# Kernel optimization log

Measured on AMD Instinct MI355X. Metric: run time of the kernel, lower is better.

Reference implementation:

```python
import jax, jax.numpy as jnp
import numpy as np

D = 128      # d_model
H = 8        # n_heads
HD = D // H  # head_dim = 16
E = 256      # n_experts
R = 32       # kv_lora_rank
B, T = 4, 512
EPS = 1e-6


def _dense_init(k, fi, fo):
    s = float(1.0 / np.sqrt(fi))
    return jax.random.uniform(k, (fi, fo), minval=-s, maxval=s, dtype=jnp.float32)


def setup_inputs() -> dict:
    key = jax.random.key(0)
    ks = jax.random.split(key, 16)
    rng = np.random.RandomState(42)
    Q, _ = np.linalg.qr(rng.randn(D, D))
    glim = float(np.sqrt(6.0 / (D + D)))
    return {
        'x': jax.random.normal(ks[0], (B, T, D), dtype=jnp.float32),
        'g1': jnp.ones((D,), jnp.float32),
        'qW': _dense_init(ks[1], D, D), 'qb': jnp.zeros((D,), jnp.float32),
        'kdW': _dense_init(ks[2], D, R), 'kdb': jnp.zeros((R,), jnp.float32),
        'kuW': _dense_init(ks[3], R, 2 * D), 'kub': jnp.zeros((2 * D,), jnp.float32),
        'oW': _dense_init(ks[4], D, D), 'ob': jnp.zeros((D,), jnp.float32),
        'rot': jnp.asarray(Q, jnp.float32),
        'tq_scale': jnp.ones((D,), jnp.float32),
        's1W': _dense_init(ks[5], D, D), 's1b': jnp.zeros((D,), jnp.float32),
        's2W': _dense_init(ks[6], D, D), 's2b': jnp.zeros((D,), jnp.float32),
        'g2': jnp.ones((D,), jnp.float32),
        'gateW': _dense_init(ks[7], D, E), 'gateb': jnp.zeros((E,), jnp.float32),
        'expW': jax.random.uniform(ks[8], (E, D, D), minval=-glim, maxval=glim, dtype=jnp.float32),
        'm1W': _dense_init(ks[9], D, D), 'm1b': jnp.zeros((D,), jnp.float32),
        'm2W': _dense_init(ks[10], D, D), 'm2b': jnp.zeros((D,), jnp.float32),
    }


def _rmsnorm(x, g):
    return g * (x / jnp.sqrt(jnp.mean(x * x, axis=-1, keepdims=True) + EPS))


def _swiglu(x, w1, b1, w2, b2):
    gate = x @ w1 + b1
    return gate * jax.nn.sigmoid(gate) * (x @ w2 + b2)


def _mla(x, qW, qb, kdW, kdb, kuW, kub, oW, ob):
    b, t = x.shape[0], x.shape[1]
    q = (x @ qW + qb).reshape(b, t, H, HD)
    kv = ((x @ kdW + kdb) @ kuW + kub).reshape(b, t, H, 2 * HD)
    k, v = jnp.split(kv, 2, axis=-1)
    q = jax.nn.elu(q) + 1.0
    k = jax.nn.elu(k) + 1.0
    # linear attention: context[b,h,d,e] = sum_t k[b,t,h,d] v[b,t,h,e]
    context = jnp.einsum('bthd,bthe->bhde', k, v)
    out = jnp.einsum('bthd,bhde->bthe', q, context)
    k_sum = jnp.sum(k, axis=1)  # [b,h,d]
    z = 1.0 / (jnp.einsum('bthd,bhd->bth', q, k_sum) + EPS)
    out = out * z[..., None]
    return out.reshape(b, t, D) @ oW + ob


def _turbo_quant(x, rot, scale):
    x = x @ rot
    mag = jnp.sqrt(jnp.mean(x * x, axis=-1, keepdims=True) + EPS)
    phase = x / mag
    qp = jnp.clip(phase * 127.0, -127.0, 127.0) / 127.0
    phase = jax.lax.stop_gradient(qp - phase) + phase  # straight-through
    return phase * mag * scale


def _moe(h, gateW, gateb, expW, m1W, m1b, m2W, m2b):
    gate_scores = jax.nn.softmax(h @ gateW + gateb, axis=-1)  # [B,T,E]
    top_vals, top_idx = jax.lax.top_k(gate_scores, 2)
    top_w = top_vals / (jnp.sum(top_vals, axis=-1, keepdims=True) + EPS)
    # dense all-expert compute as in the original module
    eo = jnp.einsum('btd,edo->bteo', h, expW)  # [B,T,E,D]
    mask = jnp.sum(jax.nn.one_hot(top_idx, E, dtype=h.dtype) * top_w[..., None], axis=2)  # [B,T,E]
    wavg = jnp.einsum('bteo,bte->bto', eo, mask)
    wavg = _swiglu(wavg, m1W, m1b, m2W, m2b)
    diff_sq = jnp.square(eo - wavg[:, :, None, :])
    wvar = jnp.einsum('bteo,bte->bto', diff_sq, mask)
    consensus = jnp.exp(-jnp.mean(wvar, axis=-1))  # [B,T]
    return wavg, consensus


def reference(x, g1, qW, qb, kdW, kdb, kuW, kub, oW, ob, rot, tq_scale,
              s1W, s1b, s2W, s2b, g2, gateW, gateb, expW, m1W, m1b, m2W, m2b):
    attn_out = _turbo_quant(_mla(_rmsnorm(x, g1), qW, qb, kdW, kdb, kuW, kub, oW, ob), rot, tq_scale)
    x = x + _swiglu(attn_out, s1W, s1b, s2W, s2b)
    moe_out, consensus = _moe(_rmsnorm(x, g2), gateW, gateb, expW, m1W, m1b, m2W, m2b)
    return x + moe_out, consensus
```

## Files before the change

kernel.cpp:

```cpp
#include <hip/hip_runtime.h>
#include <hip/hip_bf16.h>
#include <math.h>

static constexpr int Dd   = 128;
static constexpr int NH   = 8;
static constexpr int NE   = 256;
static constexpr int RR   = 32;
static constexpr int TT   = 512;
static constexpr int NTOK = 2048;
static constexpr int TPB  = 4;
static constexpr int SLOTS = 256;
#define EPSF 1e-6f

__device__ __forceinline__ float elu1(float v) { return v > 0.f ? v + 1.f : expf(v); }
__device__ __forceinline__ float sigm(float v) { return 1.f / (1.f + expf(-v)); }

__global__ __launch_bounds__(512) void k_pre(
    const float* __restrict__ x, const float* __restrict__ g1,
    const float* __restrict__ qW, const float* __restrict__ qb,
    const float* __restrict__ kdW, const float* __restrict__ kdb,
    const float* __restrict__ kuW, const float* __restrict__ kub,
    float* __restrict__ qbuf, float* __restrict__ kvbuf,
    float* __restrict__ ctx, float* __restrict__ ksum, int* __restrict__ cnt) {
  const int tid = threadIdx.x;
  const int j = tid & 127, g = tid >> 7;
  const int lane = tid & 63;
  const int n0 = blockIdx.x * TPB;

  __shared__ float4 h1T[128];
  __shared__ float4 part[3][128];
  __shared__ float4 kpart[8][32];
  __shared__ float4 kdT[32];
  __shared__ float4 kupart[256];
  __shared__ float4 rtmp[2];

  if (blockIdx.x == 0) {
    for (int i = tid; i < 32 * 256; i += 512) ctx[i] = 0.f;
    ksum[tid] = 0.f;
    if (tid < 256) cnt[tid] = 0;
  }

  float xv[4];
  if (tid < 128) {
    float v[4];
#pragma unroll
    for (int t = 0; t < 4; t++) { xv[t] = x[(n0 + t) * Dd + j]; v[t] = xv[t] * xv[t]; }
#pragma unroll
    for (int o = 32; o > 0; o >>= 1) {
#pragma unroll
      for (int t = 0; t < 4; t++) v[t] += __shfl_xor(v[t], o, 64);
    }
    if (lane == 0) rtmp[tid >> 6] = make_float4(v[0], v[1], v[2], v[3]);
  }
  __syncthreads();
  if (tid < 128) {
    float g1j = g1[j];
#pragma unroll
    for (int t = 0; t < 4; t++) {
      float ss = ((const float*)&rtmp[0])[t] + ((const float*)&rtmp[1])[t];
      ((float*)&h1T[j])[t] = g1j * xv[t] * rsqrtf(ss * (1.f / 128.f) + EPSF);
    }
  }
  __syncthreads();

  {
    float a0 = 0, a1 = 0, a2 = 0, a3 = 0;
    const float* Wp = qW + (g * 32) * Dd + j;
#pragma unroll 16
    for (int i = 0; i < 32; i++) {
      float4 h4 = h1T[g * 32 + i];
      float w = Wp[i * Dd];
      a0 += h4.x * w; a1 += h4.y * w; a2 += h4.z * w; a3 += h4.w * w;
    }
    if (g) part[g - 1][j] = make_float4(a0, a1, a2, a3);
    __syncthreads();
    if (g == 0) {
      float4 p0 = part[0][j], p1 = part[1][j], p2 = part[2][j];
      float bb = qb[j];
      qbuf[(n0 + 0) * Dd + j] = elu1(a0 + p0.x + p1.x + p2.x + bb);
      qbuf[(n0 + 1) * Dd + j] = elu1(a1 + p0.y + p1.y + p2.y + bb);
      qbuf[(n0 + 2) * Dd + j] = elu1(a2 + p0.z + p1.z + p2.z + bb);
      qbuf[(n0 + 3) * Dd + j] = elu1(a3 + p0.w + p1.w + p2.w + bb);
    }
    __syncthreads();
  }

  if (tid < 256) {
    int col = tid & 31, ksp = tid >> 5;
    float a0 = 0, a1 = 0, a2 = 0, a3 = 0;
    const float* Wp = kdW + (ksp * 16) * RR + col;
#pragma unroll
    for (int i = 0; i < 16; i++) {
      float4 h4 = h1T[ksp * 16 + i];
      float w = Wp[i * RR];
      a0 += h4.x * w; a1 += h4.y * w; a2 += h4.z * w; a3 += h4.w * w;
    }
    kpart[ksp][col] = make_float4(a0, a1, a2, a3);
  }
  __syncthreads();
  if (tid < 32) {
    float bb = kdb[tid];
    float s0 = bb, s1 = bb, s2 = bb, s3 = bb;
#pragma unroll
    for (int k = 0; k < 8; k++) {
      float4 p = kpart[k][tid];
      s0 += p.x; s1 += p.y; s2 += p.z; s3 += p.w;
    }
    kdT[tid] = make_float4(s0, s1, s2, s3);
  }
  __syncthreads();

  {
    int col = tid & 255, kh = tid >> 8;
    float a0 = 0, a1 = 0, a2 = 0, a3 = 0;
    const float* Wp = kuW + (kh * 16) * 256 + col;
#pragma unroll
    for (int r = 0; r < 16; r++) {
      float4 k4 = kdT[kh * 16 + r];
      float w = Wp[r * 256];
      a0 += k4.x * w; a1 += k4.y * w; a2 += k4.z * w; a3 += k4.w * w;
    }
    if (kh) kupart[col] = make_float4(a0, a1, a2, a3);
    __syncthreads();
    if (!kh) {
      float4 p = kupart[col];
      float bb = kub[col];
      bool isk = (col & 31) < 16;
      float v0 = a0 + p.x + bb, v1 = a1 + p.y + bb, v2 = a2 + p.z + bb, v3 = a3 + p.w + bb;
      kvbuf[(n0 + 0) * 256 + col] = isk ? elu1(v0) : v0;
      kvbuf[(n0 + 1) * 256 + col] = isk ? elu1(v1) : v1;
      kvbuf[(n0 + 2) * 256 + col] = isk ? elu1(v2) : v2;
      kvbuf[(n0 + 3) * 256 + col] = isk ? elu1(v3) : v3;
    }
  }
}

__global__ __launch_bounds__(256) void k_ctx(const float* __restrict__ kv,
                                             float* __restrict__ ctx,
                                             float* __restrict__ ksum,
                                             const float* __restrict__ oW,
                                             const float* __restrict__ ob,
                                             const float* __restrict__ rot,
                                             float* __restrict__ oR,
                                             float* __restrict__ bR) {
  const int blk = blockIdx.x;
  const int tid = threadIdx.x;
  if (blk < 256) {
    const int bh = blk >> 3, c = blk & 7;
    const int b = bh >> 3, h = bh & 7;
    const int d = tid >> 4, e = tid & 15;
    __shared__ float sh[64 * 32];
#pragma unroll
    for (int r = 0; r < 8; r++) {
      int lin = r * 256 + tid;
      int tok = lin >> 5, off = lin & 31;
      sh[lin] = kv[((b * TT + c * 64 + tok) * 256) + h * 32 + off];
    }
    __syncthreads();
    float acc = 0.f, ks = 0.f;
#pragma unroll 4
    for (int t = 0; t < 64; t++) {
      float kk = sh[t * 32 + d];
      acc += kk * sh[t * 32 + 16 + e];
      ks += kk;
    }
    atomicAdd(&ctx[bh * 256 + d * 16 + e], acc);
    if (e == 0) atomicAdd(&ksum[bh * 16 + d], ks);
  } else if (blk < 320) {
    int idx = (blk - 256) * 256 + tid;
    int row = idx >> 7, col = idx & 127;
    const float* ow = oW + row * 128;
    float acc = 0.f;
#pragma unroll 8
    for (int k = 0; k < 128; k++) acc += ow[k] * rot[k * 128 + col];
    oR[row * 128 + col] = acc;
  } else {
    if (tid < 128) {
      float acc = 0.f;
#pragma unroll 8
      for (int k = 0; k < 128; k++) acc += ob[k] * rot[k * 128 + tid];
      bR[tid] = acc;
    }
  }
}

__global__ __launch_bounds__(512) void k_mid(
    const float* __restrict__ x, const float* __restrict__ qbuf,
    const float* __restrict__ ctx, const float* __restrict__ ksum,
    const float* __restrict__ oR, const float* __restrict__ bR,
    const float* __restrict__ tqs,
    const float* __restrict__ s1W, const float* __restrict__ s1b,
    const float* __restrict__ s2W, const float* __restrict__ s2b,
    const float* __restrict__ g2, const float* __restrict__ gateW,
    const float* __restrict__ gateb,
    float* __restrict__ xnbuf, float* __restrict__ h2buf,
    float* __restrict__ gw, int* __restrict__ tokslot,
    int* __restrict__ slottok, int* __restrict__ cnt) {
  const int tid = threadIdx.x;
  const int j = tid & 127, g = tid >> 7;
  const int lane = tid & 63;
  const int n0 = blockIdx.x * TPB;
  const int b = n0 >> 9;

  __shared__ float4 bufA[128], bufB[128];
  __shared__ float4 part[3][128];
  __shared__ float4 gpart[256];
  __shared__ float4 rtmp[2];
  __shared__ float wvS[4][4]; __shared__ int wiS[4][4];
  __shared__ float zS[4][4];

  float xres[4];
  if (tid < 128) {
#pragma unroll
    for (int t = 0; t < 4; t++) xres[t] = x[(n0 + t) * Dd + j];
  }

  ((float*)&bufA[j])[g] = qbuf[(n0 + g) * Dd + j];
  __syncthreads();

  if (tid < 128) {
    int h = j >> 4, e = j & 15;
    const float* cpt = ctx + (b * NH + h) * 256;
    const float* kpt = ksum + (b * NH + h) * 16;
    float num[4] = {0, 0, 0, 0}, den[4] = {0, 0, 0, 0};
#pragma unroll
    for (int d = 0; d < 16; d++) {
      float cx = cpt[d * 16 + e], ks = kpt[d];
      float4 q4 = bufA[h * 16 + d];
      num[0] += q4.x * cx; num[1] += q4.y * cx; num[2] += q4.z * cx; num[3] += q4.w * cx;
      den[0] += q4.x * ks; den[1] += q4.y * ks; den[2] += q4.z * ks; den[3] += q4.w * ks;
    }
#pragma unroll
    for (int t = 0; t < 4; t++) ((float*)&bufB[j])[t] = num[t] / (den[t] + EPSF);
  }
  __syncthreads();

  {
    float a0 = 0, a1 = 0, a2 = 0, a3 = 0;
    const float* Wp = oR + (g * 32) * Dd + j;
#pragma unroll 16
    for (int i = 0; i < 32; i++) {
      float4 h4 = bufB[g * 32 + i];
      float w = Wp[i * Dd];
      a0 += h4.x * w; a1 += h4.y * w; a2 += h4.z * w; a3 += h4.w * w;
    }
    if (g) part[g - 1][j] = make_float4(a0, a1, a2, a3);
    __syncthreads();
    float tot[4];
    if (g == 0) {
      float4 p0 = part[0][j], p1 = part[1][j], p2 = part[2][j];
      float bb = bR[j];
      tot[0] = a0 + p0.x + p1.x + p2.x + bb; tot[1] = a1 + p0.y + p1.y + p2.y + bb;
      tot[2] = a2 + p0.z + p1.z + p2.z + bb; tot[3] = a3 + p0.w + p1.w + p2.w + bb;
      float v[4];
#pragma unroll
      for (int t = 0; t < 4; t++) v[t] = tot[t] * tot[t];
#pragma unroll
      for (int o = 32; o > 0; o >>= 1) {
#pragma unroll
        for (int t = 0; t < 4; t++) v[t] += __shfl_xor(v[t], o, 64);
      }
      if (lane == 0) rtmp[tid >> 6] = make_float4(v[0], v[1], v[2], v[3]);
    }
    __syncthreads();
    if (g == 0) {
      float scj = tqs[j];
#pragma unroll
      for (int t = 0; t < 4; t++) {
        float ss = ((const float*)&rtmp[0])[t] + ((const float*)&rtmp[1])[t];
        float mag = sqrtf(ss * (1.f / 128.f) + EPSF);
        float zc = fminf(fmaxf(tot[t], -mag), mag);
        ((float*)&bufA[j])[t] = zc * scj;
      }
    }
    __syncthreads();
  }

  {
    float a0 = 0, a1 = 0, a2 = 0, a3 = 0;
    const float* Wp = (g < 2 ? s1W : s2W) + ((g & 1) * 64) * Dd + j;
#pragma unroll 16
    for (int i = 0; i < 64; i++) {
      float4 h4 = bufA[(g & 1) * 64 + i];
      float w = Wp[i * Dd];
      a0 += h4.x * w; a1 += h4.y * w; a2 += h4.z * w; a3 += h4.w * w;
    }
    if (g) part[g - 1][j] = make_float4(a0, a1, a2, a3);
    __syncthreads();
    if (g == 0) {
      float b1 = s1b[j], b2 = s2b[j];
      float4 p0 = part[0][j], p1 = part[1][j], p2 = part[2][j];
      float gv[4], uv[4], xn[4], v[4];
      gv[0] = a0 + p0.x + b1; gv[1] = a1 + p0.y + b1;
      gv[2] = a2 + p0.z + b1; gv[3] = a3 + p0.w + b1;
      uv[0] = p1.x + p2.x + b2; uv[1] = p1.y + p2.y + b2;
      uv[2] = p1.z + p2.z + b2; uv[3] = p1.w + p2.w + b2;
      float g2j = g2[j];
#pragma unroll
      for (int t = 0; t < 4; t++) {
        xn[t] = xres[t] + gv[t] * sigm(gv[t]) * uv[t];
        xnbuf[(n0 + t) * Dd + j] = xn[t];
        ((float*)&bufB[j])[t] = g2j * xn[t];
        v[t] = xn[t] * xn[t];
      }
#pragma unroll
      for (int o = 32; o > 0; o >>= 1) {
#pragma unroll
        for (int t = 0; t < 4; t++) v[t] += __shfl_xor(v[t], o, 64);
      }
      if (lane == 0) rtmp[tid >> 6] = make_float4(v[0], v[1], v[2], v[3]);
    }
    __syncthreads();
  }

  float val[4];
  float r2[4];
  {
    int col = tid & 255, kh = tid >> 8;
    float a0 = 0, a1 = 0, a2 = 0, a3 = 0;
    const float* Wp = gateW + (kh * 64) * NE + col;
#pragma unroll 16
    for (int i = 0; i < 64; i++) {
      float4 h4 = bufB[kh * 64 + i];
      float w = Wp[i * NE];
      a0 += h4.x * w; a1 += h4.y * w; a2 += h4.z * w; a3 += h4.w * w;
    }
    if (kh) gpart[col] = make_float4(a0, a1, a2, a3);
    __syncthreads();
#pragma unroll
    for (int t = 0; t < 4; t++) {
      float ss = ((const float*)&rtmp[0])[t] + ((const float*)&rtmp[1])[t];
      r2[t] = rsqrtf(ss * (1.f / 128.f) + EPSF);
    }
    if (!kh) {
      float4 p = gpart[col];
      float bb = gateb[col];
      val[0] = (a0 + p.x) * r2[0] + bb; val[1] = (a1 + p.y) * r2[1] + bb;
      val[2] = (a2 + p.z) * r2[2] + bb; val[3] = (a3 + p.w) * r2[3] + bb;
    }
    if (tid < 128) {
#pragma unroll
      for (int t = 0; t < 4; t++)
        h2buf[(n0 + t) * Dd + j] = ((const float*)&bufB[j])[t] * r2[t];
    }
  }
  __syncthreads();

  float m1[4]; int i1[4];
  {
    if (tid < 256) {
      float bv[4]; int bi[4];
#pragma unroll
      for (int t = 0; t < 4; t++) { bv[t] = val[t]; bi[t] = tid; }
#pragma unroll
      for (int o = 32; o > 0; o >>= 1) {
#pragma unroll
        for (int t = 0; t < 4; t++) {
          float wv = __shfl_xor(bv[t], o, 64);
          int wi = __shfl_xor(bi[t], o, 64);
          if (wv > bv[t] || (wv == bv[t] && wi < bi[t])) { bv[t] = wv; bi[t] = wi; }
        }
      }
      if (lane == 0) {
#pragma unroll
        for (int t = 0; t < 4; t++) { wvS[tid >> 6][t] = bv[t]; wiS[tid >> 6][t] = bi[t]; }
      }
    }
    __syncthreads();
    if (tid < 256) {
#pragma unroll
      for (int t = 0; t < 4; t++) {
        m1[t] = wvS[0][t]; i1[t] = wiS[0][t];
#pragma unroll
        for (int w = 1; w < 4; w++) {
          float cv = wvS[w][t]; int ci = wiS[w][t];
          if (cv > m1[t] || (cv == m1[t] && ci < i1[t])) { m1[t] = cv; i1[t] = ci; }
        }
      }
    }
    __syncthreads();
  }
  float m2[4]; int i2[4];
  {
    if (tid < 256) {
      float bv[4]; int bi[4];
#pragma unroll
      for (int t = 0; t < 4; t++) {
        bv[t] = (tid == i1[t]) ? -INFINITY : val[t];
        bi[t] = tid;
      }
#pragma unroll
      for (int o = 32; o > 0; o >>= 1) {
#pragma unroll
        for (int t = 0; t < 4; t++) {
          float wv = __shfl_xor(bv[t], o, 64);
          int wi = __shfl_xor(bi[t], o, 64);
          if (wv > bv[t] || (wv == bv[t] && wi < bi[t])) { bv[t] = wv; bi[t] = wi; }
        }
      }
      if (lane == 0) {
#pragma unroll
        for (int t = 0; t < 4; t++) { wvS[tid >> 6][t] = bv[t]; wiS[tid >> 6][t] = bi[t]; }
      }
    }
    __syncthreads();
    if (tid < 256) {
#pragma unroll
      for (int t = 0; t < 4; t++) {
        m2[t] = wvS[0][t]; i2[t] = wiS[0][t];
#pragma unroll
        for (int w = 1; w < 4; w++) {
          float cv = wvS[w][t]; int ci = wiS[w][t];
          if (cv > m2[t] || (cv == m2[t] && ci < i2[t])) { m2[t] = cv; i2[t] = ci; }
        }
      }
    }
    __syncthreads();
  }
  {
    if (tid < 256) {
      float v[4];
#pragma unroll
      for (int t = 0; t < 4; t++) v[t] = expf(val[t] - m1[t]);
#pragma unroll
      for (int o = 32; o > 0; o >>= 1) {
#pragma unroll
        for (int t = 0; t < 4; t++) v[t] += __shfl_xor(v[t], o, 64);
      }
      if (lane == 0) {
#pragma unroll
        for (int t = 0; t < 4; t++) zS[tid >> 6][t] = v[t];
      }
    }
    __syncthreads();
  }
  if (tid < 4) {
    int t = tid, tok = n0 + t;
    float Z = zS[0][t] + zS[1][t] + zS[2][t] + zS[3][t];
    float p1 = 1.f / Z;
    float p2 = expf(m2[t] - m1[t]) / Z;
    float s = p1 + p2 + EPSF;
    int e1 = i1[t], e2 = i2[t];
    int s1 = atomicAdd(&cnt[e1], 1); if (s1 > SLOTS - 1) s1 = SLOTS - 1;
    int s2 = atomicAdd(&cnt[e2], 1); if (s2 > SLOTS - 1) s2 = SLOTS - 1;
    int sl1 = e1 * SLOTS + s1, sl2 = e2 * SLOTS + s2;
    slottok[sl1] = tok; slottok[sl2] = tok;
    tokslot[tok * 2] = sl1; tokslot[tok * 2 + 1] = sl2;
    gw[tok * 2] = p1 / s; gw[tok * 2 + 1] = p2 / s;
  }
}

__global__ __launch_bounds__(512) void k_exp(const float* __restrict__ h2buf,
                                             const int* __restrict__ slottok,
                                             const int* __restrict__ cnt,
                                             const float* __restrict__ expW,
                                             float* __restrict__ ybuf) {
  const int e = blockIdx.x;
  int n = cnt[e]; if (n > SLOTS) n = SLOTS;
  if (n == 0) return;
  const int base = e * SLOTS;
  const int tid = threadIdx.x;
  const int j = tid & 127, g = tid >> 7;
  __shared__ __align__(16) float hT[128 * 20];
  const float* Wp = expW + (size_t)e * Dd * Dd + j;
  for (int t0 = 0; t0 < n; t0 += 16) {
    int m = n - t0; if (m > 16) m = 16;
    __syncthreads();
    for (int tt = g; tt < m; tt += 4) {
      int tok = slottok[base + t0 + tt];
      hT[j * 20 + tt] = h2buf[tok * Dd + j];
    }
    __syncthreads();
    float acc[4] = {0, 0, 0, 0};
#pragma unroll 8
    for (int i = 0; i < 128; i++) {
      float w = Wp[i * Dd];
      float4 h4 = *(const float4*)&hT[i * 20 + g * 4];
      acc[0] += h4.x * w; acc[1] += h4.y * w; acc[2] += h4.z * w; acc[3] += h4.w * w;
    }
#pragma unroll
    for (int k = 0; k < 4; k++) {
      int tt = g * 4 + k;
      if (tt < m) ybuf[(size_t)(base + t0 + tt) * Dd + j] = acc[k];
    }
  }
}

__global__ __launch_bounds__(512) void k_post(
    const float* __restrict__ xnbuf, const float* __restrict__ ybuf,
    const int* __restrict__ tokslot, const float* __restrict__ gw,
    const float* __restrict__ m1W, const float* __restrict__ m1b,
    const float* __restrict__ m2W, const float* __restrict__ m2b,
    float* __restrict__ out) {
  const int tid = threadIdx.x;
  const int j = tid & 127, g = tid >> 7;
  const int lane = tid & 63;
  const int n0 = blockIdx.x * TPB;

  __shared__ float4 y1T[128], y2T[128], inT[128], sT[128];
  __shared__ float4 part[3][128];
  __shared__ float4 rtmp[2];
  __shared__ int sSlot[4][2];
  __shared__ float sWt[4][2];

  if (tid < 4) {
    sSlot[tid][0] = tokslot[(n0 + tid) * 2];
    sSlot[tid][1] = tokslot[(n0 + tid) * 2 + 1];
    sWt[tid][0] = gw[(n0 + tid) * 2];
    sWt[tid][1] = gw[(n0 + tid) * 2 + 1];
  }
  __syncthreads();

  {
    float y1 = ybuf[(size_t)sSlot[g][0] * Dd + j];
    float y2 = ybuf[(size_t)sSlot[g][1] * Dd + j];
    ((float*)&y1T[j])[g] = y1;
    ((float*)&y2T[j])[g] = y2;
    ((float*)&inT[j])[g] = sWt[g][0] * y1 + sWt[g][1] * y2;
  }
  __syncthreads();

  {
    float a0 = 0, a1 = 0, a2 = 0, a3 = 0;
    const float* Wp = (g < 2 ? m1W : m2W) + ((g & 1) * 64) * Dd + j;
#pragma unroll 16
    for (int i = 0; i < 64; i++) {
      float4 h4 = inT[(g & 1) * 64 + i];
      float w = Wp[i * Dd];
      a0 += h4.x * w; a1 += h4.y * w; a2 += h4.z * w; a3 += h4.w * w;
    }
    if (g) part[g - 1][j] = make_float4(a0, a1, a2, a3);
    __syncthreads();
    if (g == 0) {
      float b1 = m1b[j], b2 = m2b[j];
      float4 p0 = part[0][j], p1 = part[1][j], p2 = part[2][j];
      float gv[4], uv[4];
      gv[0] = a0 + p0.x + b1; gv[1] = a1 + p0.y + b1;
      gv[2] = a2 + p0.z + b1; gv[3] = a3 + p0.w + b1;
      uv[0] = p1.x + p2.x + b2; uv[1] = p1.y + p2.y + b2;
      uv[2] = p1.z + p2.z + b2; uv[3] = p1.w + p2.w + b2;
#pragma unroll
      for (int t = 0; t < 4; t++) {
        float sv = gv[t] * sigm(gv[t]) * uv[t];
        ((float*)&sT[j])[t] = sv;
        out[(n0 + t) * Dd + j] = xnbuf[(n0 + t) * Dd + j] + sv;
      }
    }
    __syncthreads();
  }

  if (tid < 128) {
    float v[4];
#pragma unroll
    for (int t = 0; t < 4; t++) {
      float sv = ((const float*)&sT[j])[t];
      float d1 = ((const float*)&y1T[j])[t] - sv;
      float d2 = ((const float*)&y2T[j])[t] - sv;
      v[t] = sWt[t][0] * d1 * d1 + sWt[t][1] * d2 * d2;
    }
#pragma unroll
    for (int o = 32; o > 0; o >>= 1) {
#pragma unroll
      for (int t = 0; t < 4; t++) v[t] += __shfl_xor(v[t], o, 64);
    }
    if (lane == 0) rtmp[tid >> 6] = make_float4(v[0], v[1], v[2], v[3]);
  }
  __syncthreads();
  if (tid < 4) {
    float s = ((const float*)&rtmp[0])[tid] + ((const float*)&rtmp[1])[tid];
    out[NTOK * Dd + n0 + tid] = expf(-s * (1.f / 128.f));
  }
}

extern "C" void kernel_launch(void* const* d_in, const int* in_sizes, int n_in,
                              void* d_out, int out_size, void* d_ws, size_t ws_size,
                              hipStream_t stream) {
  const float* x   = (const float*)d_in[0];
  const float* g1  = (const float*)d_in[1];
  const float* qW  = (const float*)d_in[2];
  const float* qb  = (const float*)d_in[3];
  const float* kdW = (const float*)d_in[4];
  const float* kdb = (const float*)d_in[5];
  const float* kuW = (const float*)d_in[6];
  const float* kub = (const float*)d_in[7];
  const float* oW  = (const float*)d_in[8];
  const float* ob  = (const float*)d_in[9];
  const float* rot = (const float*)d_in[10];
  const float* tqs = (const float*)d_in[11];
  const float* s1W = (const float*)d_in[12];
  const float* s1b = (const float*)d_in[13];
  const float* s2W = (const float*)d_in[14];
  const float* s2b = (const float*)d_in[15];
  const float* g2  = (const float*)d_in[16];
  const float* gW  = (const float*)d_in[17];
  const float* gb  = (const float*)d_in[18];
  const float* eW  = (const float*)d_in[19];
  const float* m1W = (const float*)d_in[20];
  const float* m1b = (const float*)d_in[21];
  const float* m2W = (const float*)d_in[22];
  const float* m2b = (const float*)d_in[23];
  float* out = (float*)d_out;
  float* ws  = (float*)d_ws;

  float* qbuf   = ws;
  float* kvbuf  = ws + 262144;
  float* ctx    = ws + 786432;
  float* ksum   = ws + 794624;
  float* h2buf  = ws + 795136;
  float* xnbuf  = ws + 1057280;
  float* gw     = ws + 1319424;
  float* oRb    = ws + 1323520;
  float* bRb    = ws + 1339904;
  int*   cnt     = (int*)(ws + 1373056);
  int*   tokslot = (int*)(ws + 1373312);
  int*   slottok = (int*)(ws + 1377408);
  float* ybuf   = ws + 1442944;

  k_pre<<<NTOK / TPB, 512, 0, stream>>>(x, g1, qW, qb, kdW, kdb, kuW, kub,
                                        qbuf, kvbuf, ctx, ksum, cnt);
  k_ctx<<<321, 256, 0, stream>>>(kvbuf, ctx, ksum, oW, ob, rot, oRb, bRb);
  k_mid<<<NTOK / TPB, 512, 0, stream>>>(x, qbuf, ctx, ksum, oRb, bRb, tqs,
                                        s1W, s1b, s2W, s2b, g2, gW, gb,
                                        xnbuf, h2buf, gw, tokslot, slottok, cnt);
  k_exp<<<NE, 512, 0, stream>>>(h2buf, slottok, cnt, eW, ybuf);
  k_post<<<NTOK / TPB, 512, 0, stream>>>(xnbuf, ybuf, tokslot, gw,
                                         m1W, m1b, m2W, m2b, out);
}
```

Measured before the change: 165.4 us.

## Fuse pipeline into two stages with per-token expert compute and in-block context accumulation

Five kernels become a zero kernel plus two fused stages. The linear-attention context and key sums are now accumulated with atomics straight from each block's K/V in shared memory, so the kvbuf round trip and the separate ctx kernel go away. The oW·rot precompute also moves into stage1. The MoE top-2 expert matmuls now run inside stage2 per 4-token block, loading weights by token instead of grouping tokens by expert. This drops the slot-scatter bookkeeping, the expert and post kernels, and the h2/xn/y buffers, but each block rereads full expert weight matrices with less reuse and issues many more atomics.

```diff
diff --git a/kernel.cpp b/kernel.cpp
--- a/kernel.cpp
+++ b/kernel.cpp
@@ -1,31 +1,38 @@
 #include <hip/hip_runtime.h>
-#include <hip/hip_bf16.h>
 #include <math.h>
 
-static constexpr int Dd   = 128;
-static constexpr int NH   = 8;
-static constexpr int NE   = 256;
-static constexpr int RR   = 32;
-static constexpr int TT   = 512;
-static constexpr int NTOK = 2048;
-static constexpr int TPB  = 4;
-static constexpr int SLOTS = 256;
+static constexpr int Dd    = 128;
+static constexpr int NH    = 8;
+static constexpr int NE    = 256;
+static constexpr int RR    = 32;
+static constexpr int NTOK  = 2048;
 #define EPSF 1e-6f
 
 __device__ __forceinline__ float elu1(float v) { return v > 0.f ? v + 1.f : expf(v); }
 __device__ __forceinline__ float sigm(float v) { return 1.f / (1.f + expf(-v)); }
 
-__global__ __launch_bounds__(512) void k_pre(
+__global__ __launch_bounds__(512) void k_zero(float* __restrict__ ctx,
+                                              float* __restrict__ ksum) {
+  int idx = blockIdx.x * 512 + threadIdx.x;
+  if (idx < 8192) ctx[idx] = 0.f;
+  else if (idx < 8704) ksum[idx - 8192] = 0.f;
+}
+
+__global__ __launch_bounds__(512) void k_stage1(
     const float* __restrict__ x, const float* __restrict__ g1,
     const float* __restrict__ qW, const float* __restrict__ qb,
     const float* __restrict__ kdW, const float* __restrict__ kdb,
     const float* __restrict__ kuW, const float* __restrict__ kub,
-    float* __restrict__ qbuf, float* __restrict__ kvbuf,
-    float* __restrict__ ctx, float* __restrict__ ksum, int* __restrict__ cnt) {
+    const float* __restrict__ oW, const float* __restrict__ ob,
+    const float* __restrict__ rot,
+    float* __restrict__ qbuf, float* __restrict__ ctx, float* __restrict__ ksum,
+    float* __restrict__ oR, float* __restrict__ bR) {
   const int tid = threadIdx.x;
+  const int bid = blockIdx.x;
   const int j = tid & 127, g = tid >> 7;
   const int lane = tid & 63;
-  const int n0 = blockIdx.x * TPB;
+  const int n0 = bid * 4;
+  const int b = bid >> 7;
 
   __shared__ float4 h1T[128];
   __shared__ float4 part[3][128];
@@ -33,12 +40,8 @@
   __shared__ float4 kdT[32];
   __shared__ float4 kupart[256];
   __shared__ float4 rtmp[2];
-
-  if (blockIdx.x == 0) {
-    for (int i = tid; i < 32 * 256; i += 512) ctx[i] = 0.f;
-    ksum[tid] = 0.f;
-    if (tid < 256) cnt[tid] = 0;
-  }
+  __shared__ __align__(16) float kS[8][16][4];
+  __shared__ __align__(16) float vS[8][16][4];
 
   float xv[4];
   if (tid < 128) {
@@ -125,66 +128,52 @@
     if (!kh) {
       float4 p = kupart[col];
       float bb = kub[col];
-      bool isk = (col & 31) < 16;
       float v0 = a0 + p.x + bb, v1 = a1 + p.y + bb, v2 = a2 + p.z + bb, v3 = a3 + p.w + bb;
-      kvbuf[(n0 + 0) * 256 + col] = isk ? elu1(v0) : v0;
-      kvbuf[(n0 + 1) * 256 + col] = isk ? elu1(v1) : v1;
-      kvbuf[(n0 + 2) * 256 + col] = isk ? elu1(v2) : v2;
-      kvbuf[(n0 + 3) * 256 + col] = isk ? elu1(v3) : v3;
-    }
-  }
-}
-
-__global__ __launch_bounds__(256) void k_ctx(const float* __restrict__ kv,
-                                             float* __restrict__ ctx,
-                                             float* __restrict__ ksum,
-                                             const float* __restrict__ oW,
-                                             const float* __restrict__ ob,
-                                             const float* __restrict__ rot,
-                                             float* __restrict__ oR,
-                                             float* __restrict__ bR) {
-  const int blk = blockIdx.x;
-  const int tid = threadIdx.x;
-  if (blk < 256) {
-    const int bh = blk >> 3, c = blk & 7;
-    const int b = bh >> 3, h = bh & 7;
-    const int d = tid >> 4, e = tid & 15;
-    __shared__ float sh[64 * 32];
-#pragma unroll
-    for (int r = 0; r < 8; r++) {
-      int lin = r * 256 + tid;
-      int tok = lin >> 5, off = lin & 31;
-      sh[lin] = kv[((b * TT + c * 64 + tok) * 256) + h * 32 + off];
-    }
-    __syncthreads();
-    float acc = 0.f, ks = 0.f;
-#pragma unroll 4
-    for (int t = 0; t < 64; t++) {
-      float kk = sh[t * 32 + d];
-      acc += kk * sh[t * 32 + 16 + e];
-      ks += kk;
-    }
-    atomicAdd(&ctx[bh * 256 + d * 16 + e], acc);
-    if (e == 0) atomicAdd(&ksum[bh * 16 + d], ks);
-  } else if (blk < 320) {
-    int idx = (blk - 256) * 256 + tid;
+      int h = col >> 5, off = col & 31;
+      if (off < 16) {
+        kS[h][off][0] = elu1(v0); kS[h][off][1] = elu1(v1);
+        kS[h][off][2] = elu1(v2); kS[h][off][3] = elu1(v3);
+      } else {
+        vS[h][off - 16][0] = v0; vS[h][off - 16][1] = v1;
+        vS[h][off - 16][2] = v2; vS[h][off - 16][3] = v3;
+      }
+    }
+  }
+  __syncthreads();
+
+  {
+    const int h = tid >> 6;
+    const int d = (tid >> 2) & 15;
+    const int e0 = (tid & 3) * 4;
+    const int bh = b * NH + h;
+    float4 k4 = *(const float4*)&kS[h][d][0];
+    float* cp = ctx + bh * 256 + d * 16 + e0;
+#pragma unroll
+    for (int ee = 0; ee < 4; ee++) {
+      float4 v4 = *(const float4*)&vS[h][e0 + ee][0];
+      atomicAdd(cp + ee, k4.x * v4.x + k4.y * v4.y + k4.z * v4.z + k4.w * v4.w);
+    }
+    if ((tid & 3) == 0)
+      atomicAdd(&ksum[bh * 16 + d], k4.x + k4.y + k4.z + k4.w);
+  }
+
+  if (bid < 32) {
+    int idx = bid * 512 + tid;
     int row = idx >> 7, col = idx & 127;
     const float* ow = oW + row * 128;
     float acc = 0.f;
 #pragma unroll 8
     for (int k = 0; k < 128; k++) acc += ow[k] * rot[k * 128 + col];
-    oR[row * 128 + col] = acc;
-  } else {
-    if (tid < 128) {
-      float acc = 0.f;
+    oR[idx] = acc;
+  } else if (bid == 32 && tid < 128) {
+    float acc = 0.f;
 #pragma unroll 8
-      for (int k = 0; k < 128; k++) acc += ob[k] * rot[k * 128 + tid];
-      bR[tid] = acc;
-    }
+    for (int k = 0; k < 128; k++) acc += ob[k] * rot[k * 128 + tid];
+    bR[tid] = acc;
   }
 }
 
-__global__ __launch_bounds__(512) void k_mid(
+__global__ __launch_bounds__(512) void k_stage2(
     const float* __restrict__ x, const float* __restrict__ qbuf,
     const float* __restrict__ ctx, const float* __restrict__ ksum,
     const float* __restrict__ oR, const float* __restrict__ bR,
@@ -192,14 +181,14 @@
     const float* __restrict__ s1W, const float* __restrict__ s1b,
     const float* __restrict__ s2W, const float* __restrict__ s2b,
     const float* __restrict__ g2, const float* __restrict__ gateW,
-    const float* __restrict__ gateb,
-    float* __restrict__ xnbuf, float* __restrict__ h2buf,
-    float* __restrict__ gw, int* __restrict__ tokslot,
-    int* __restrict__ slottok, int* __restrict__ cnt) {
+    const float* __restrict__ gateb, const float* __restrict__ expW,
+    const float* __restrict__ m1W, const float* __restrict__ m1b,
+    const float* __restrict__ m2W, const float* __restrict__ m2b,
+    float* __restrict__ out) {
   const int tid = threadIdx.x;
   const int j = tid & 127, g = tid >> 7;
   const int lane = tid & 63;
-  const int n0 = blockIdx.x * TPB;
+  const int n0 = blockIdx.x * 4;
   const int b = n0 >> 9;
 
   __shared__ float4 bufA[128], bufB[128];
@@ -208,6 +197,11 @@
   __shared__ float4 rtmp[2];
   __shared__ float wvS[4][4]; __shared__ int wiS[4][4];
   __shared__ float zS[4][4];
+  __shared__ float sWt[4][2]; __shared__ int sE[4][2];
+  __shared__ float h2T[128][4];
+  __shared__ float epS[8][4][128];
+  __shared__ float yT[8][128];
+  __shared__ float4 inT[128], sT[128];
 
   float xres[4];
   if (tid < 128) {
@@ -276,6 +270,7 @@
     __syncthreads();
   }
 
+  float xn[4] = {0.f, 0.f, 0.f, 0.f};
   {
     float a0 = 0, a1 = 0, a2 = 0, a3 = 0;
     const float* Wp = (g < 2 ? s1W : s2W) + ((g & 1) * 64) * Dd + j;
@@ -290,7 +285,7 @@
     if (g == 0) {
       float b1 = s1b[j], b2 = s2b[j];
       float4 p0 = part[0][j], p1 = part[1][j], p2 = part[2][j];
-      float gv[4], uv[4], xn[4], v[4];
+      float gv[4], uv[4], v[4];
       gv[0] = a0 + p0.x + b1; gv[1] = a1 + p0.y + b1;
       gv[2] = a2 + p0.z + b1; gv[3] = a3 + p0.w + b1;
       uv[0] = p1.x + p2.x + b2; uv[1] = p1.y + p2.y + b2;
@@ -299,7 +294,6 @@
 #pragma unroll
       for (int t = 0; t < 4; t++) {
         xn[t] = xres[t] + gv[t] * sigm(gv[t]) * uv[t];
-        xnbuf[(n0 + t) * Dd + j] = xn[t];
         ((float*)&bufB[j])[t] = g2j * xn[t];
         v[t] = xn[t] * xn[t];
       }
@@ -313,8 +307,7 @@
     __syncthreads();
   }
 
-  float val[4];
-  float r2[4];
+  float val[4]; float r2v[4];
   {
     int col = tid & 255, kh = tid >> 8;
     float a0 = 0, a1 = 0, a2 = 0, a3 = 0;
@@ -330,18 +323,18 @@
 #pragma unroll
     for (int t = 0; t < 4; t++) {
       float ss = ((const float*)&rtmp[0])[t] + ((const float*)&rtmp[1])[t];
-      r2[t] = rsqrtf(ss * (1.f / 128.f) + EPSF);
+      r2v[t] = rsqrtf(ss * (1.f / 128.f) + EPSF);
     }
     if (!kh) {
       float4 p = gpart[col];
       float bb = gateb[col];
-      val[0] = (a0 + p.x) * r2[0] + bb; val[1] = (a1 + p.y) * r2[1] + bb;
-      val[2] = (a2 + p.z) * r2[2] + bb; val[3] = (a3 + p.w) * r2[3] + bb;
+      val[0] = (a0 + p.x) * r2v[0] + bb; val[1] = (a1 + p.y) * r2v[1] + bb;
+      val[2] = (a2 + p.z) * r2v[2] + bb; val[3] = (a3 + p.w) * r2v[3] + bb;
     }
     if (tid < 128) {
 #pragma unroll
       for (int t = 0; t < 4; t++)
-        h2buf[(n0 + t) * Dd + j] = ((const float*)&bufB[j])[t] * r2[t];
+        h2T[j][t] = ((const float*)&bufB[j])[t] * r2v[t];
     }
   }
   __syncthreads();
@@ -435,87 +428,48 @@
     __syncthreads();
   }
   if (tid < 4) {
-    int t = tid, tok = n0 + t;
+    int t = tid;
     float Z = zS[0][t] + zS[1][t] + zS[2][t] + zS[3][t];
     float p1 = 1.f / Z;
     float p2 = expf(m2[t] - m1[t]) / Z;
     float s = p1 + p2 + EPSF;
-    int e1 = i1[t], e2 = i2[t];
-    int s1 = atomicAdd(&cnt[e1], 1); if (s1 > SLOTS - 1) s1 = SLOTS - 1;
-    int s2 = atomicAdd(&cnt[e2], 1); if (s2 > SLOTS - 1) s2 = SLOTS - 1;
-    int sl1 = e1 * SLOTS + s1, sl2 = e2 * SLOTS + s2;
-    slottok[sl1] = tok; slottok[sl2] = tok;
-    tokslot[tok * 2] = sl1; tokslot[tok * 2 + 1] = sl2;
-    gw[tok * 2] = p1 / s; gw[tok * 2 + 1] = p2 / s;
-  }
-}
-
-__global__ __launch_bounds__(512) void k_exp(const float* __restrict__ h2buf,
-                                             const int* __restrict__ slottok,
-                                             const int* __restrict__ cnt,
-                                             const float* __restrict__ expW,
-                                             float* __restrict__ ybuf) {
-  const int e = blockIdx.x;
-  int n = cnt[e]; if (n > SLOTS) n = SLOTS;
-  if (n == 0) return;
-  const int base = e * SLOTS;
-  const int tid = threadIdx.x;
-  const int j = tid & 127, g = tid >> 7;
-  __shared__ __align__(16) float hT[128 * 20];
-  const float* Wp = expW + (size_t)e * Dd * Dd + j;
-  for (int t0 = 0; t0 < n; t0 += 16) {
-    int m = n - t0; if (m > 16) m = 16;
-    __syncthreads();
-    for (int tt = g; tt < m; tt += 4) {
-      int tok = slottok[base + t0 + tt];
-      hT[j * 20 + tt] = h2buf[tok * Dd + j];
-    }
-    __syncthreads();
-    float acc[4] = {0, 0, 0, 0};
-#pragma unroll 8
-    for (int i = 0; i < 128; i++) {
-      float w = Wp[i * Dd];
-      float4 h4 = *(const float4*)&hT[i * 20 + g * 4];
-      acc[0] += h4.x * w; acc[1] += h4.y * w; acc[2] += h4.z * w; acc[3] += h4.w * w;
-    }
-#pragma unroll
-    for (int k = 0; k < 4; k++) {
-      int tt = g * 4 + k;
-      if (tt < m) ybuf[(size_t)(base + t0 + tt) * Dd + j] = acc[k];
-    }
-  }
-}
-
-__global__ __launch_bounds__(512) void k_post(
-    const float* __restrict__ xnbuf, const float* __restrict__ ybuf,
-    const int* __restrict__ tokslot, const float* __restrict__ gw,
-    const float* __restrict__ m1W, const float* __restrict__ m1b,
-    const float* __restrict__ m2W, const float* __restrict__ m2b,
-    float* __restrict__ out) {
-  const int tid = threadIdx.x;
-  const int j = tid & 127, g = tid >> 7;
-  const int lane = tid & 63;
-  const int n0 = blockIdx.x * TPB;
-
-  __shared__ float4 y1T[128], y2T[128], inT[128], sT[128];
-  __shared__ float4 part[3][128];
-  __shared__ float4 rtmp[2];
-  __shared__ int sSlot[4][2];
-  __shared__ float sWt[4][2];
-
-  if (tid < 4) {
-    sSlot[tid][0] = tokslot[(n0 + tid) * 2];
-    sSlot[tid][1] = tokslot[(n0 + tid) * 2 + 1];
-    sWt[tid][0] = gw[(n0 + tid) * 2];
-    sWt[tid][1] = gw[(n0 + tid) * 2 + 1];
-  }
-  __syncthreads();
-
-  {
-    float y1 = ybuf[(size_t)sSlot[g][0] * Dd + j];
-    float y2 = ybuf[(size_t)sSlot[g][1] * Dd + j];
-    ((float*)&y1T[j])[g] = y1;
-    ((float*)&y2T[j])[g] = y2;
+    sE[t][0] = i1[t]; sE[t][1] = i2[t];
+    sWt[t][0] = p1 / s; sWt[t][1] = p2 / s;
+  }
+  __syncthreads();
+
+  {
+    const float* wb[8];
+#pragma unroll
+    for (int p = 0; p < 8; p++) {
+      int e = sE[p >> 1][p & 1];
+      wb[p] = expW + (size_t)e * (Dd * Dd) + (g * 32) * Dd + j;
+    }
+    float acc[8] = {0, 0, 0, 0, 0, 0, 0, 0};
+#pragma unroll 4
+    for (int i = 0; i < 32; i++) {
+      float hv[4];
+#pragma unroll
+      for (int t = 0; t < 4; t++) hv[t] = h2T[g * 32 + i][t];
+#pragma unroll
+      for (int p = 0; p < 8; p++) acc[p] += wb[p][i * Dd] * hv[p >> 1];
+    }
+#pragma unroll
+    for (int p = 0; p < 8; p++) epS[p][g][j] = acc[p];
+  }
+  __syncthreads();
+  {
+#pragma unroll
+    for (int r = 0; r < 2; r++) {
+      int p = r * 4 + g;
+      yT[p][j] = epS[p][0][j] + epS[p][1][j] + epS[p][2][j] + epS[p][3][j];
+    }
+  }
+  __syncthreads();
+
+  {
+    float y1 = yT[g * 2 + 0][j];
+    float y2 = yT[g * 2 + 1][j];
     ((float*)&inT[j])[g] = sWt[g][0] * y1 + sWt[g][1] * y2;
   }
   __syncthreads();
@@ -543,7 +497,7 @@
       for (int t = 0; t < 4; t++) {
         float sv = gv[t] * sigm(gv[t]) * uv[t];
         ((float*)&sT[j])[t] = sv;
-        out[(n0 + t) * Dd + j] = xnbuf[(n0 + t) * Dd + j] + sv;
+        out[(n0 + t) * Dd + j] = xn[t] + sv;
       }
     }
     __syncthreads();
@@ -554,8 +508,8 @@
 #pragma unroll
     for (int t = 0; t < 4; t++) {
       float sv = ((const float*)&sT[j])[t];
-      float d1 = ((const float*)&y1T[j])[t] - sv;
-      float d2 = ((const float*)&y2T[j])[t] - sv;
+      float d1 = yT[t * 2 + 0][j] - sv;
+      float d2 = yT[t * 2 + 1][j] - sv;
       v[t] = sWt[t][0] * d1 * d1 + sWt[t][1] * d2 * d2;
     }
 #pragma unroll
@@ -602,27 +556,16 @@
   float* out = (float*)d_out;
   float* ws  = (float*)d_ws;
 
-  float* qbuf   = ws;
-  float* kvbuf  = ws + 262144;
-  float* ctx    = ws + 786432;
-  float* ksum   = ws + 794624;
-  float* h2buf  = ws + 795136;
-  float* xnbuf  = ws + 1057280;
-  float* gw     = ws + 1319424;
-  float* oRb    = ws + 1323520;
-  float* bRb    = ws + 1339904;
-  int*   cnt     = (int*)(ws + 1373056);
-  int*   tokslot = (int*)(ws + 1373312);
-  int*   slottok = (int*)(ws + 1377408);
-  float* ybuf   = ws + 1442944;
-
-  k_pre<<<NTOK / TPB, 512, 0, stream>>>(x, g1, qW, qb, kdW, kdb, kuW, kub,
-                                        qbuf, kvbuf, ctx, ksum, cnt);
-  k_ctx<<<321, 256, 0, stream>>>(kvbuf, ctx, ksum, oW, ob, rot, oRb, bRb);
-  k_mid<<<NTOK / TPB, 512, 0, stream>>>(x, qbuf, ctx, ksum, oRb, bRb, tqs,
-                                        s1W, s1b, s2W, s2b, g2, gW, gb,
-                                        xnbuf, h2buf, gw, tokslot, slottok, cnt);
-  k_exp<<<NE, 512, 0, stream>>>(h2buf, slottok, cnt, eW, ybuf);
-  k_post<<<NTOK / TPB, 512, 0, stream>>>(xnbuf, ybuf, tokslot, gw,
+  float* ctx  = ws;
+  float* ksum = ws + 8192;
+  float* oR   = ws + 8704;
+  float* bR   = ws + 25088;
+  float* qbuf = ws + 25216;
+
+  k_zero<<<17, 512, 0, stream>>>(ctx, ksum);
+  k_stage1<<<NTOK / 4, 512, 0, stream>>>(x, g1, qW, qb, kdW, kdb, kuW, kub,
+                                         oW, ob, rot, qbuf, ctx, ksum, oR, bR);
+  k_stage2<<<NTOK / 4, 512, 0, stream>>>(x, qbuf, ctx, ksum, oR, bR, tqs,
+                                         s1W, s1b, s2W, s2b, g2, gW, gb, eW,
                                          m1W, m1b, m2W, m2b, out);
 }
```

Measured after the change: 197.9 us. 19.7% more time.

## Fuse linear-attention context into k_pre with replicated atomic partials, split expert blocks

Applied to the files above, without the earlier changes.

The per-token k/v outer products are now accumulated directly inside k_pre from shared memory into 16 replicated partial context buffers using atomics. A small reduction kernel then sums the replicas. This removes the kvbuf round trip through global memory and the separate k_ctx pass. The oW·rot precompute moves into k_pre, zeroing moves into a dedicated kernel, and k_exp now launches two blocks per expert that take alternating 16-token chunks. In exchange there are many more atomics, two extra small launches, and a launch for every expert block even when that expert has no tokens.

```diff
diff --git a/kernel.cpp b/kernel.cpp
--- a/kernel.cpp
+++ b/kernel.cpp
@@ -1,31 +1,42 @@
 #include <hip/hip_runtime.h>
-#include <hip/hip_bf16.h>
 #include <math.h>
 
-static constexpr int Dd   = 128;
-static constexpr int NH   = 8;
-static constexpr int NE   = 256;
-static constexpr int RR   = 32;
-static constexpr int TT   = 512;
-static constexpr int NTOK = 2048;
-static constexpr int TPB  = 4;
+static constexpr int Dd    = 128;
+static constexpr int NH    = 8;
+static constexpr int NE    = 256;
+static constexpr int RR    = 32;
+static constexpr int NTOK  = 2048;
 static constexpr int SLOTS = 256;
+static constexpr int NCPY  = 16;
 #define EPSF 1e-6f
 
 __device__ __forceinline__ float elu1(float v) { return v > 0.f ? v + 1.f : expf(v); }
 __device__ __forceinline__ float sigm(float v) { return 1.f / (1.f + expf(-v)); }
+
+__global__ __launch_bounds__(512) void k_zero(float* __restrict__ ctxp,
+                                              float* __restrict__ ksump,
+                                              int* __restrict__ cnt) {
+  int idx = blockIdx.x * 512 + threadIdx.x;
+  if (idx < NCPY * 8192) ctxp[idx] = 0.f;
+  else if (idx < NCPY * 8192 + NCPY * 512) ksump[idx - NCPY * 8192] = 0.f;
+  else if (idx < NCPY * 8192 + NCPY * 512 + NE) cnt[idx - NCPY * 8192 - NCPY * 512] = 0;
+}
 
 __global__ __launch_bounds__(512) void k_pre(
     const float* __restrict__ x, const float* __restrict__ g1,
     const float* __restrict__ qW, const float* __restrict__ qb,
     const float* __restrict__ kdW, const float* __restrict__ kdb,
     const float* __restrict__ kuW, const float* __restrict__ kub,
-    float* __restrict__ qbuf, float* __restrict__ kvbuf,
-    float* __restrict__ ctx, float* __restrict__ ksum, int* __restrict__ cnt) {
+    const float* __restrict__ oW, const float* __restrict__ ob,
+    const float* __restrict__ rot,
+    float* __restrict__ qbuf, float* __restrict__ ctxp, float* __restrict__ ksump,
+    float* __restrict__ oR, float* __restrict__ bR) {
   const int tid = threadIdx.x;
+  const int bid = blockIdx.x;
   const int j = tid & 127, g = tid >> 7;
   const int lane = tid & 63;
-  const int n0 = blockIdx.x * TPB;
+  const int n0 = bid * 4;
+  const int b = bid >> 7;
 
   __shared__ float4 h1T[128];
   __shared__ float4 part[3][128];
@@ -33,12 +44,8 @@
   __shared__ float4 kdT[32];
   __shared__ float4 kupart[256];
   __shared__ float4 rtmp[2];
-
-  if (blockIdx.x == 0) {
-    for (int i = tid; i < 32 * 256; i += 512) ctx[i] = 0.f;
-    ksum[tid] = 0.f;
-    if (tid < 256) cnt[tid] = 0;
-  }
+  __shared__ __align__(16) float kS[8][16][4];
+  __shared__ __align__(16) float vS[8][16][4];
 
   float xv[4];
   if (tid < 128) {
@@ -125,62 +132,68 @@
     if (!kh) {
       float4 p = kupart[col];
       float bb = kub[col];
-      bool isk = (col & 31) < 16;
       float v0 = a0 + p.x + bb, v1 = a1 + p.y + bb, v2 = a2 + p.z + bb, v3 = a3 + p.w + bb;
-      kvbuf[(n0 + 0) * 256 + col] = isk ? elu1(v0) : v0;
-      kvbuf[(n0 + 1) * 256 + col] = isk ? elu1(v1) : v1;
-      kvbuf[(n0 + 2) * 256 + col] = isk ? elu1(v2) : v2;
-      kvbuf[(n0 + 3) * 256 + col] = isk ? elu1(v3) : v3;
-    }
-  }
-}
-
-__global__ __launch_bounds__(256) void k_ctx(const float* __restrict__ kv,
-                                             float* __restrict__ ctx,
-                                             float* __restrict__ ksum,
-                                             const float* __restrict__ oW,
-                                             const float* __restrict__ ob,
-                                             const float* __restrict__ rot,
-                                             float* __restrict__ oR,
-                                             float* __restrict__ bR) {
-  const int blk = blockIdx.x;
-  const int tid = threadIdx.x;
-  if (blk < 256) {
-    const int bh = blk >> 3, c = blk & 7;
-    const int b = bh >> 3, h = bh & 7;
-    const int d = tid >> 4, e = tid & 15;
-    __shared__ float sh[64 * 32];
-#pragma unroll
-    for (int r = 0; r < 8; r++) {
-      int lin = r * 256 + tid;
-      int tok = lin >> 5, off = lin & 31;
-      sh[lin] = kv[((b * TT + c * 64 + tok) * 256) + h * 32 + off];
-    }
-    __syncthreads();
-    float acc = 0.f, ks = 0.f;
-#pragma unroll 4
-    for (int t = 0; t < 64; t++) {
-      float kk = sh[t * 32 + d];
-      acc += kk * sh[t * 32 + 16 + e];
-      ks += kk;
-    }
-    atomicAdd(&ctx[bh * 256 + d * 16 + e], acc);
-    if (e == 0) atomicAdd(&ksum[bh * 16 + d], ks);
-  } else if (blk < 320) {
-    int idx = (blk - 256) * 256 + tid;
+      int h = col >> 5, off = col & 31;
+      if (off < 16) {
+        kS[h][off][0] = elu1(v0); kS[h][off][1] = elu1(v1);
+        kS[h][off][2] = elu1(v2); kS[h][off][3] = elu1(v3);
+      } else {
+        vS[h][off - 16][0] = v0; vS[h][off - 16][1] = v1;
+        vS[h][off - 16][2] = v2; vS[h][off - 16][3] = v3;
+      }
+    }
+  }
+  __syncthreads();
+
+  {
+    const int h = tid >> 6;
+    const int d = (tid >> 2) & 15;
+    const int e0 = (tid & 3) * 4;
+    const int bh = b * NH + h;
+    const int cpy = bid & (NCPY - 1);
+    float4 k4 = *(const float4*)&kS[h][d][0];
+    float* cp = ctxp + (cpy * 32 + bh) * 256 + d * 16 + e0;
+#pragma unroll
+    for (int ee = 0; ee < 4; ee++) {
+      float4 v4 = *(const float4*)&vS[h][e0 + ee][0];
+      atomicAdd(cp + ee, k4.x * v4.x + k4.y * v4.y + k4.z * v4.z + k4.w * v4.w);
+    }
+    if ((tid & 3) == 0)
+      atomicAdd(&ksump[(cpy * 32 + bh) * 16 + d], k4.x + k4.y + k4.z + k4.w);
+  }
+
+  if (bid < 32) {
+    int idx = bid * 512 + tid;
     int row = idx >> 7, col = idx & 127;
     const float* ow = oW + row * 128;
     float acc = 0.f;
 #pragma unroll 8
     for (int k = 0; k < 128; k++) acc += ow[k] * rot[k * 128 + col];
-    oR[row * 128 + col] = acc;
-  } else {
-    if (tid < 128) {
-      float acc = 0.f;
+    oR[idx] = acc;
+  } else if (bid == 32 && tid < 128) {
+    float acc = 0.f;
 #pragma unroll 8
-      for (int k = 0; k < 128; k++) acc += ob[k] * rot[k * 128 + tid];
-      bR[tid] = acc;
-    }
+    for (int k = 0; k < 128; k++) acc += ob[k] * rot[k * 128 + tid];
+    bR[tid] = acc;
+  }
+}
+
+__global__ __launch_bounds__(512) void k_redc(const float* __restrict__ ctxp,
+                                              const float* __restrict__ ksump,
+                                              float* __restrict__ ctx,
+                                              float* __restrict__ ksum) {
+  int idx = blockIdx.x * 512 + threadIdx.x;
+  if (idx < 8192) {
+    float s = 0.f;
+#pragma unroll
+    for (int c = 0; c < NCPY; c++) s += ctxp[c * 8192 + idx];
+    ctx[idx] = s;
+  } else if (idx < 8704) {
+    int i2 = idx - 8192;
+    float s = 0.f;
+#pragma unroll
+    for (int c = 0; c < NCPY; c++) s += ksump[c * 512 + i2];
+    ksum[i2] = s;
   }
 }
 
@@ -199,7 +212,7 @@
   const int tid = threadIdx.x;
   const int j = tid & 127, g = tid >> 7;
   const int lane = tid & 63;
-  const int n0 = blockIdx.x * TPB;
+  const int n0 = blockIdx.x * 4;
   const int b = n0 >> 9;
 
   __shared__ float4 bufA[128], bufB[128];
@@ -455,15 +468,14 @@
                                              const int* __restrict__ cnt,
                                              const float* __restrict__ expW,
                                              float* __restrict__ ybuf) {
-  const int e = blockIdx.x;
+  const int e = blockIdx.x >> 1, sub = blockIdx.x & 1;
   int n = cnt[e]; if (n > SLOTS) n = SLOTS;
-  if (n == 0) return;
   const int base = e * SLOTS;
   const int tid = threadIdx.x;
   const int j = tid & 127, g = tid >> 7;
   __shared__ __align__(16) float hT[128 * 20];
   const float* Wp = expW + (size_t)e * Dd * Dd + j;
-  for (int t0 = 0; t0 < n; t0 += 16) {
+  for (int t0 = sub * 16; t0 < n; t0 += 32) {
     int m = n - t0; if (m > 16) m = 16;
     __syncthreads();
     for (int tt = g; tt < m; tt += 4) {
@@ -495,7 +507,7 @@
   const int tid = threadIdx.x;
   const int j = tid & 127, g = tid >> 7;
   const int lane = tid & 63;
-  const int n0 = blockIdx.x * TPB;
+  const int n0 = blockIdx.x * 4;
 
   __shared__ float4 y1T[128], y2T[128], inT[128], sT[128];
   __shared__ float4 part[3][128];
@@ -602,27 +614,29 @@
   float* out = (float*)d_out;
   float* ws  = (float*)d_ws;
 
-  float* qbuf   = ws;
-  float* kvbuf  = ws + 262144;
-  float* ctx    = ws + 786432;
-  float* ksum   = ws + 794624;
-  float* h2buf  = ws + 795136;
-  float* xnbuf  = ws + 1057280;
-  float* gw     = ws + 1319424;
-  float* oRb    = ws + 1323520;
-  float* bRb    = ws + 1339904;
-  int*   cnt     = (int*)(ws + 1373056);
-  int*   tokslot = (int*)(ws + 1373312);
-  int*   slottok = (int*)(ws + 1377408);
-  float* ybuf   = ws + 1442944;
-
-  k_pre<<<NTOK / TPB, 512, 0, stream>>>(x, g1, qW, qb, kdW, kdb, kuW, kub,
-                                        qbuf, kvbuf, ctx, ksum, cnt);
-  k_ctx<<<321, 256, 0, stream>>>(kvbuf, ctx, ksum, oW, ob, rot, oRb, bRb);
-  k_mid<<<NTOK / TPB, 512, 0, stream>>>(x, qbuf, ctx, ksum, oRb, bRb, tqs,
-                                        s1W, s1b, s2W, s2b, g2, gW, gb,
-                                        xnbuf, h2buf, gw, tokslot, slottok, cnt);
-  k_exp<<<NE, 512, 0, stream>>>(h2buf, slottok, cnt, eW, ybuf);
-  k_post<<<NTOK / TPB, 512, 0, stream>>>(xnbuf, ybuf, tokslot, gw,
-                                         m1W, m1b, m2W, m2b, out);
+  float* ctxp    = ws;
+  float* ksump   = ws + 131072;
+  float* ctx     = ws + 139264;
+  float* ksum    = ws + 147456;
+  float* oR      = ws + 147968;
+  float* bR      = ws + 164352;
+  float* qbuf    = ws + 164480;
+  float* xnbuf   = ws + 426624;
+  float* h2buf   = ws + 688768;
+  float* gw      = ws + 950912;
+  int*   cnt     = (int*)(ws + 955008);
+  int*   tokslot = (int*)(ws + 955264);
+  int*   slottok = (int*)(ws + 959360);
+  float* ybuf    = ws + 1024896;
+
+  k_zero<<<273, 512, 0, stream>>>(ctxp, ksump, cnt);
+  k_pre<<<NTOK / 4, 512, 0, stream>>>(x, g1, qW, qb, kdW, kdb, kuW, kub,
+                                      oW, ob, rot, qbuf, ctxp, ksump, oR, bR);
+  k_redc<<<17, 512, 0, stream>>>(ctxp, ksump, ctx, ksum);
+  k_mid<<<NTOK / 4, 512, 0, stream>>>(x, qbuf, ctx, ksum, oR, bR, tqs,
+                                      s1W, s1b, s2W, s2b, g2, gW, gb,
+                                      xnbuf, h2buf, gw, tokslot, slottok, cnt);
+  k_exp<<<NE * 2, 512, 0, stream>>>(h2buf, slottok, cnt, eW, ybuf);
+  k_post<<<NTOK / 4, 512, 0, stream>>>(xnbuf, ybuf, tokslot, gw,
+                                       m1W, m1b, m2W, m2b, out);
 }
```

Measured after the change: 184.8 us. +11.7%, slower.
